# Performance work log

Hardware: AMD Instinct MI355X
Metric: run time of the kernel (lower is better)

## Reference

```python
import jax, jax.numpy as jnp
import numpy as np

N = 8192
IN_F = 256
OUT_F = 128


def setup_inputs() -> dict:
    key = jax.random.key(0)
    k1, k2, k3, k4, k5, k6 = jax.random.split(key, 6)
    input = jax.random.normal(k1, (N, IN_F), dtype=jnp.float32)
    adj = jax.random.randint(k2, (N, N), 0, 2, dtype=jnp.int32)
    # xavier-uniform-like init scaled by gain=0.5
    def xavier(k, shape, gain=0.5):
        fan_in, fan_out = shape[0], shape[1]
        lim = gain * np.sqrt(6.0 / (fan_in + fan_out))
        return jax.random.uniform(k, shape, dtype=jnp.float32, minval=-lim, maxval=lim)
    W_s = xavier(k3, (IN_F, OUT_F))
    a_s = xavier(k4, (OUT_F, 1))
    W_n = xavier(k5, (IN_F, OUT_F))
    a_n = xavier(k6, (OUT_F, 1))
    return {"input": input, "adj": adj, "W_s": W_s, "a_s": a_s, "W_n": W_n, "a_n": a_n}


def reference(input, adj, W_s, a_s, W_n, a_n):
    # Projections: [N, out_features]
    h_s = input @ W_s
    h_n = input @ W_n
    # Additive attention logits: e[i, j] = relu((h_s @ a_s)[i] + (h_n @ a_n)[j])
    e = jax.nn.relu((h_s @ a_s) + (h_n @ a_n).T)  # [N, N]
    # Masked softmax over neighbors (dim=1)
    attention = jnp.where(adj > 0, e, jnp.float32(-9e15))
    attention = jax.nn.softmax(attention, axis=1)
    # Self-scaling term (sum of softmax rows, kept for faithfulness)
    attention_sum = jnp.sum(attention, axis=-1, keepdims=True)
    attention_s = 1.0 / (1.0 + attention_sum)
    # Dropout is identity in eval mode (p=0 / training=False)
    h_prime = attention_s * h_s + attention @ h_n
    # concat=True -> elu activation
    return jax.nn.elu(h_prime)
```

## Files before the change

### kernel.cpp

```cpp
#include <hip/hip_runtime.h>
#include <math.h>

#define NN 8192

typedef short short8 __attribute__((ext_vector_type(8)));
typedef float f32x4 __attribute__((ext_vector_type(4)));

__device__ __forceinline__ float eluf(float x) {
  return x > 0.f ? x : (__expf(x) - 1.f);
}
__device__ __forceinline__ unsigned short f2bf(float f) {
  union { float f; unsigned u; } v; v.f = f;
  unsigned r = v.u + 0x7fffu + ((v.u >> 16) & 1u);
  return (unsigned short)(r >> 16);
}

__global__ __launch_bounds__(256) void k_proj(const float* __restrict__ X,
                                              const float* __restrict__ Ws,
                                              const float* __restrict__ Wn,
                                              const float* __restrict__ as_,
                                              const float* __restrict__ an_,
                                              float* __restrict__ Hs,
                                              unsigned short* __restrict__ HnT,
                                              float* __restrict__ s_out,
                                              float* __restrict__ n_out) {
  __shared__ float4 lin4[8 * 64];
  const int t = threadIdx.x;
  const int i0 = blockIdx.x * 8;
  const float4* Xg = (const float4*)X + (size_t)i0 * 64;
  lin4[t] = Xg[t];
  if (t < 256) lin4[t + 256] = Xg[t + 256];
  __syncthreads();
  const int c = t & 127;
  const int rh = t >> 7;
  float accs[4], accn[4];
#pragma unroll
  for (int r = 0; r < 4; ++r) { accs[r] = 0.f; accn[r] = 0.f; }
  for (int k = 0; k < 256; k += 4) {
    float ws0 = Ws[(k + 0) * 128 + c], ws1 = Ws[(k + 1) * 128 + c];
    float ws2 = Ws[(k + 2) * 128 + c], ws3 = Ws[(k + 3) * 128 + c];
    float wn0 = Wn[(k + 0) * 128 + c], wn1 = Wn[(k + 1) * 128 + c];
    float wn2 = Wn[(k + 2) * 128 + c], wn3 = Wn[(k + 3) * 128 + c];
#pragma unroll
    for (int r = 0; r < 4; ++r) {
      float4 iv = lin4[(rh * 4 + r) * 64 + (k >> 2)];
      accs[r] = fmaf(iv.x, ws0, accs[r]); accs[r] = fmaf(iv.y, ws1, accs[r]);
      accs[r] = fmaf(iv.z, ws2, accs[r]); accs[r] = fmaf(iv.w, ws3, accs[r]);
      accn[r] = fmaf(iv.x, wn0, accn[r]); accn[r] = fmaf(iv.y, wn1, accn[r]);
      accn[r] = fmaf(iv.z, wn2, accn[r]); accn[r] = fmaf(iv.w, wn3, accn[r]);
    }
  }
#pragma unroll
  for (int r = 0; r < 4; ++r)
    Hs[(size_t)(i0 + rh * 4 + r) * 128 + c] = accs[r];
  {
    union { unsigned short us[4]; ushort4 u4; } pk;
#pragma unroll
    for (int r = 0; r < 4; ++r) pk.us[r] = f2bf(accn[r]);
    *(ushort4*)(HnT + (size_t)c * NN + i0 + rh * 4) = pk.u4;
  }
  float* red = (float*)lin4;
  const int wv = t >> 6, ln = t & 63;
  __syncthreads();
  {
    float av = as_[c];
#pragma unroll
    for (int r = 0; r < 4; ++r) red[(rh * 4 + r) * 128 + c] = accs[r] * av;
  }
  __syncthreads();
#pragma unroll
  for (int h = 0; h < 2; ++h) {
    int row = wv * 2 + h;
    float p = red[row * 128 + ln] + red[row * 128 + 64 + ln];
#pragma unroll
    for (int off = 32; off >= 1; off >>= 1) p += __shfl_down(p, off);
    if (ln == 0) s_out[i0 + row] = p;
  }
  __syncthreads();
  {
    float av = an_[c];
#pragma unroll
    for (int r = 0; r < 4; ++r) red[(rh * 4 + r) * 128 + c] = accn[r] * av;
  }
  __syncthreads();
#pragma unroll
  for (int h = 0; h < 2; ++h) {
    int row = wv * 2 + h;
    float p = red[row * 128 + ln] + red[row * 128 + 64 + ln];
#pragma unroll
    for (int off = 32; off >= 1; off >>= 1) p += __shfl_down(p, off);
    if (ln == 0) n_out[i0 + row] = p;
  }
}

__global__ __launch_bounds__(256) void k_main(const int* __restrict__ A,
                                              const unsigned short* __restrict__ HnT,
                                              const float* __restrict__ sv_g,
                                              const float* __restrict__ nv_g,
                                              float* __restrict__ HsOut) {
  __shared__ short8 fragbuf[2][4][64];
  __shared__ float zsh[64];
  __shared__ float zf[16];

  const int t = threadIdx.x;
  const int wv = t >> 6;
  const int ln = t & 63;
  const int q = ln >> 4;
  const int m = ln & 15;
  const int row0 = blockIdx.x * 16;

  const float sm = sv_g[row0 + m];
  const int jlane = wv * 32 + q * 8;
  const int* aptr = A + (size_t)(row0 + m) * NN + jlane;
  const float* nptr = nv_g + jlane;

  const int f0 = wv * 32 + m;
  const unsigned short* bb0 = HnT + (size_t)f0 * NN + q * 8;
  const unsigned short* bb1 = HnT + (size_t)(f0 + 16) * NN + q * 8;

  f32x4 acc0 = {0.f, 0.f, 0.f, 0.f}, acc1 = {0.f, 0.f, 0.f, 0.f};
  float zp = 0.f;

  int4 adjv[2][2];
  float4 nvv[2][2];
  union { uint4 u; short8 s; } breg[8];
  adjv[0][0] = *(const int4*)(aptr);       adjv[0][1] = *(const int4*)(aptr + 4);
  adjv[1][0] = *(const int4*)(aptr + 128); adjv[1][1] = *(const int4*)(aptr + 132);
  nvv[0][0] = *(const float4*)(nptr);      nvv[0][1] = *(const float4*)(nptr + 4);
  breg[0].u = *(const uint4*)(bb0);        breg[1].u = *(const uint4*)(bb0 + 32);
  breg[2].u = *(const uint4*)(bb0 + 64);   breg[3].u = *(const uint4*)(bb0 + 96);
  breg[4].u = *(const uint4*)(bb1);        breg[5].u = *(const uint4*)(bb1 + 32);
  breg[6].u = *(const uint4*)(bb1 + 64);   breg[7].u = *(const uint4*)(bb1 + 96);

#pragma unroll 2
  for (int tt = 0; tt < 64; ++tt) {
    const int cur = tt & 1;
    {
      float nvl[8] = {nvv[cur][0].x, nvv[cur][0].y, nvv[cur][0].z, nvv[cur][0].w,
                      nvv[cur][1].x, nvv[cur][1].y, nvv[cur][1].z, nvv[cur][1].w};
      int av[8] = {adjv[cur][0].x, adjv[cur][0].y, adjv[cur][0].z, adjv[cur][0].w,
                   adjv[cur][1].x, adjv[cur][1].y, adjv[cur][1].z, adjv[cur][1].w};
      short8 fr;
#pragma unroll
      for (int k = 0; k < 8; ++k) {
        float w = av[k] > 0 ? __expf(fmaxf(sm + nvl[k], 0.f)) : 0.f;
        zp += w;
        fr[k] = (short)f2bf(w);
      }
      fragbuf[cur][wv][ln] = fr;
    }
    if (tt < 62) {
      const int* p = aptr + (tt + 2) * 128;
      adjv[cur][0] = *(const int4*)p;
      adjv[cur][1] = *(const int4*)(p + 4);
    }
    if (tt < 63) {
      const float* p = nptr + (tt + 1) * 128;
      nvv[cur ^ 1][0] = *(const float4*)p;
      nvv[cur ^ 1][1] = *(const float4*)(p + 4);
    }
    __syncthreads();
    short8 a0 = fragbuf[cur][0][ln];
    short8 a1 = fragbuf[cur][1][ln];
    short8 a2 = fragbuf[cur][2][ln];
    short8 a3 = fragbuf[cur][3][ln];
    acc0 = __builtin_amdgcn_mfma_f32_16x16x32_bf16(a0, breg[0].s, acc0, 0, 0, 0);
    acc1 = __builtin_amdgcn_mfma_f32_16x16x32_bf16(a0, breg[4].s, acc1, 0, 0, 0);
    acc0 = __builtin_amdgcn_mfma_f32_16x16x32_bf16(a1, breg[1].s, acc0, 0, 0, 0);
    acc1 = __builtin_amdgcn_mfma_f32_16x16x32_bf16(a1, breg[5].s, acc1, 0, 0, 0);
    acc0 = __builtin_amdgcn_mfma_f32_16x16x32_bf16(a2, breg[2].s, acc0, 0, 0, 0);
    acc1 = __builtin_amdgcn_mfma_f32_16x16x32_bf16(a2, breg[6].s, acc1, 0, 0, 0);
    acc0 = __builtin_amdgcn_mfma_f32_16x16x32_bf16(a3, breg[3].s, acc0, 0, 0, 0);
    acc1 = __builtin_amdgcn_mfma_f32_16x16x32_bf16(a3, breg[7].s, acc1, 0, 0, 0);
    if (tt < 63) {
      const size_t jt = (size_t)(tt + 1) * 128;
      breg[0].u = *(const uint4*)(bb0 + jt);      breg[1].u = *(const uint4*)(bb0 + jt + 32);
      breg[2].u = *(const uint4*)(bb0 + jt + 64); breg[3].u = *(const uint4*)(bb0 + jt + 96);
      breg[4].u = *(const uint4*)(bb1 + jt);      breg[5].u = *(const uint4*)(bb1 + jt + 32);
      breg[6].u = *(const uint4*)(bb1 + jt + 64); breg[7].u = *(const uint4*)(bb1 + jt + 96);
    }
  }

  {
    float zz = zp;
    zz += __shfl_down(zz, 32);
    zz += __shfl_down(zz, 16);
    if (ln < 16) zsh[wv * 16 + ln] = zz;
  }
  __syncthreads();
  if (t < 16) zf[t] = 1.f / (zsh[t] + zsh[16 + t] + zsh[32 + t] + zsh[48 + t]);
  __syncthreads();

#pragma unroll
  for (int reg = 0; reg < 4; ++reg) {
    const int row = q * 4 + reg;
    const float invz = zf[row];
    const size_t off = (size_t)(row0 + row) * 128 + f0;
    float h0 = HsOut[off], h1 = HsOut[off + 16];
    HsOut[off]      = eluf(fmaf(acc0[reg], invz, 0.5f * h0));
    HsOut[off + 16] = eluf(fmaf(acc1[reg], invz, 0.5f * h1));
  }
}

extern "C" void kernel_launch(void* const* d_in, const int* in_sizes, int n_in,
                              void* d_out, int out_size, void* d_ws, size_t ws_size,
                              hipStream_t stream) {
  const float* X   = (const float*)d_in[0];
  const int*   A   = (const int*)d_in[1];
  const float* Ws  = (const float*)d_in[2];
  const float* as_ = (const float*)d_in[3];
  const float* Wn  = (const float*)d_in[4];
  const float* an_ = (const float*)d_in[5];
  float* out = (float*)d_out;

  unsigned short* HnT = (unsigned short*)d_ws;
  float* s = (float*)(HnT + (size_t)128 * NN);
  float* n = s + NN;

  k_proj<<<1024, 256, 0, stream>>>(X, Ws, Wn, as_, an_, out, HnT, s, n);
  k_main<<<512, 256, 0, stream>>>(A, HnT, s, n, out);
}
```

Baseline: 464.6 us.

## Split neighbor dimension across waves with blocked HnT layout and LDS reduction

The attention-times-Hn product is now split along the neighbor (K) dimension instead of the feature dimension. Each of 8 waves covers a contiguous 1024-column slice of adj and computes all 128 output features with its own attention fragment, so the per-iteration LDS exchange and __syncthreads are gone. HnT is rewritten into a blocked 8-element-chunk layout so B-fragment loads are contiguous. Partial accumulators are then reduced across waves through a 64KB LDS buffer, and the block grows to 512 threads with s_setprio around the MFMAs. In exchange it uses more registers (8 accumulators) and a large LDS footprint that may limit occupancy.

```diff
diff --git a/kernel.cpp b/kernel.cpp
--- a/kernel.cpp
+++ b/kernel.cpp
@@ -57,7 +57,7 @@
     union { unsigned short us[4]; ushort4 u4; } pk;
 #pragma unroll
     for (int r = 0; r < 4; ++r) pk.us[r] = f2bf(accn[r]);
-    *(ushort4*)(HnT + (size_t)c * NN + i0 + rh * 4) = pk.u4;
+    *(ushort4*)(HnT + (size_t)blockIdx.x * 1024 + c * 8 + rh * 4) = pk.u4;
   }
   float* red = (float*)lin4;
   const int wv = t >> 6, ln = t & 63;
@@ -93,13 +93,13 @@
   }
 }
 
-__global__ __launch_bounds__(256) void k_main(const int* __restrict__ A,
-                                              const unsigned short* __restrict__ HnT,
-                                              const float* __restrict__ sv_g,
-                                              const float* __restrict__ nv_g,
-                                              float* __restrict__ HsOut) {
-  __shared__ short8 fragbuf[2][4][64];
-  __shared__ float zsh[64];
+__global__ __launch_bounds__(512, 4) void k_main(const int* __restrict__ A,
+                                                 const unsigned short* __restrict__ HnT,
+                                                 const float* __restrict__ sv_g,
+                                                 const float* __restrict__ nv_g,
+                                                 float* __restrict__ HsOut) {
+  __shared__ float accbuf[8][16][128];
+  __shared__ float zsh[8][16];
   __shared__ float zf[16];
 
   const int t = threadIdx.x;
@@ -110,74 +110,71 @@
   const int row0 = blockIdx.x * 16;
 
   const float sm = sv_g[row0 + m];
-  const int jlane = wv * 32 + q * 8;
-  const int* aptr = A + (size_t)(row0 + m) * NN + jlane;
-  const float* nptr = nv_g + jlane;
-
-  const int f0 = wv * 32 + m;
-  const unsigned short* bb0 = HnT + (size_t)f0 * NN + q * 8;
-  const unsigned short* bb1 = HnT + (size_t)(f0 + 16) * NN + q * 8;
-
-  f32x4 acc0 = {0.f, 0.f, 0.f, 0.f}, acc1 = {0.f, 0.f, 0.f, 0.f};
+  const int jbase = wv * 1024 + q * 8;
+  const int* aptr = A + (size_t)(row0 + m) * NN + jbase;
+  const float* nptr = nv_g + jbase;
+  const unsigned short* bptr = HnT + ((size_t)(wv * 128 + q) * 128 + m) * 8;
+
+  f32x4 acc[8];
+#pragma unroll
+  for (int ft = 0; ft < 8; ++ft) acc[ft] = (f32x4){0.f, 0.f, 0.f, 0.f};
   float zp = 0.f;
 
   int4 adjv[2][2];
   float4 nvv[2][2];
-  union { uint4 u; short8 s; } breg[8];
+  union Breg { uint4 u; short8 s; };
+  Breg breg[8];
+
   adjv[0][0] = *(const int4*)(aptr);       adjv[0][1] = *(const int4*)(aptr + 4);
-  adjv[1][0] = *(const int4*)(aptr + 128); adjv[1][1] = *(const int4*)(aptr + 132);
+  adjv[1][0] = *(const int4*)(aptr + 32);  adjv[1][1] = *(const int4*)(aptr + 36);
   nvv[0][0] = *(const float4*)(nptr);      nvv[0][1] = *(const float4*)(nptr + 4);
-  breg[0].u = *(const uint4*)(bb0);        breg[1].u = *(const uint4*)(bb0 + 32);
-  breg[2].u = *(const uint4*)(bb0 + 64);   breg[3].u = *(const uint4*)(bb0 + 96);
-  breg[4].u = *(const uint4*)(bb1);        breg[5].u = *(const uint4*)(bb1 + 32);
-  breg[6].u = *(const uint4*)(bb1 + 64);   breg[7].u = *(const uint4*)(bb1 + 96);
+  breg[0].u = *(const uint4*)(bptr);       breg[1].u = *(const uint4*)(bptr + 128);
+  breg[2].u = *(const uint4*)(bptr + 256); breg[3].u = *(const uint4*)(bptr + 384);
+  breg[4].u = *(const uint4*)(bptr + 512); breg[5].u = *(const uint4*)(bptr + 640);
+  breg[6].u = *(const uint4*)(bptr + 768); breg[7].u = *(const uint4*)(bptr + 896);
 
 #pragma unroll 2
-  for (int tt = 0; tt < 64; ++tt) {
+  for (int tt = 0; tt < 32; ++tt) {
     const int cur = tt & 1;
+    short8 fr;
     {
       float nvl[8] = {nvv[cur][0].x, nvv[cur][0].y, nvv[cur][0].z, nvv[cur][0].w,
                       nvv[cur][1].x, nvv[cur][1].y, nvv[cur][1].z, nvv[cur][1].w};
       int av[8] = {adjv[cur][0].x, adjv[cur][0].y, adjv[cur][0].z, adjv[cur][0].w,
                    adjv[cur][1].x, adjv[cur][1].y, adjv[cur][1].z, adjv[cur][1].w};
-      short8 fr;
 #pragma unroll
       for (int k = 0; k < 8; ++k) {
         float w = av[k] > 0 ? __expf(fmaxf(sm + nvl[k], 0.f)) : 0.f;
         zp += w;
         fr[k] = (short)f2bf(w);
       }
-      fragbuf[cur][wv][ln] = fr;
-    }
-    if (tt < 62) {
-      const int* p = aptr + (tt + 2) * 128;
+    }
+    if (tt < 31) {
+      const float* p = nptr + (tt + 1) * 32;
+      nvv[cur ^ 1][0] = *(const float4*)p;
+      nvv[cur ^ 1][1] = *(const float4*)(p + 4);
+    }
+    __builtin_amdgcn_s_setprio(1);
+    acc[0] = __builtin_amdgcn_mfma_f32_16x16x32_bf16(fr, breg[0].s, acc[0], 0, 0, 0);
+    acc[1] = __builtin_amdgcn_mfma_f32_16x16x32_bf16(fr, breg[1].s, acc[1], 0, 0, 0);
+    acc[2] = __builtin_amdgcn_mfma_f32_16x16x32_bf16(fr, breg[2].s, acc[2], 0, 0, 0);
+    acc[3] = __builtin_amdgcn_mfma_f32_16x16x32_bf16(fr, breg[3].s, acc[3], 0, 0, 0);
+    acc[4] = __builtin_amdgcn_mfma_f32_16x16x32_bf16(fr, breg[4].s, acc[4], 0, 0, 0);
+    acc[5] = __builtin_amdgcn_mfma_f32_16x16x32_bf16(fr, breg[5].s, acc[5], 0, 0, 0);
+    acc[6] = __builtin_amdgcn_mfma_f32_16x16x32_bf16(fr, breg[6].s, acc[6], 0, 0, 0);
+    acc[7] = __builtin_amdgcn_mfma_f32_16x16x32_bf16(fr, breg[7].s, acc[7], 0, 0, 0);
+    __builtin_amdgcn_s_setprio(0);
+    if (tt < 31) {
+      const unsigned short* p = bptr + (size_t)(tt + 1) * 4096;
+      breg[0].u = *(const uint4*)(p);       breg[1].u = *(const uint4*)(p + 128);
+      breg[2].u = *(const uint4*)(p + 256); breg[3].u = *(const uint4*)(p + 384);
+      breg[4].u = *(const uint4*)(p + 512); breg[5].u = *(const uint4*)(p + 640);
+      breg[6].u = *(const uint4*)(p + 768); breg[7].u = *(const uint4*)(p + 896);
+    }
+    if (tt < 30) {
+      const int* p = aptr + (tt + 2) * 32;
       adjv[cur][0] = *(const int4*)p;
       adjv[cur][1] = *(const int4*)(p + 4);
-    }
-    if (tt < 63) {
-      const float* p = nptr + (tt + 1) * 128;
-      nvv[cur ^ 1][0] = *(const float4*)p;
-      nvv[cur ^ 1][1] = *(const float4*)(p + 4);
-    }
-    __syncthreads();
-    short8 a0 = fragbuf[cur][0][ln];
-    short8 a1 = fragbuf[cur][1][ln];
-    short8 a2 = fragbuf[cur][2][ln];
-    short8 a3 = fragbuf[cur][3][ln];
-    acc0 = __builtin_amdgcn_mfma_f32_16x16x32_bf16(a0, breg[0].s, acc0, 0, 0, 0);
-    acc1 = __builtin_amdgcn_mfma_f32_16x16x32_bf16(a0, breg[4].s, acc1, 0, 0, 0);
-    acc0 = __builtin_amdgcn_mfma_f32_16x16x32_bf16(a1, breg[1].s, acc0, 0, 0, 0);
-    acc1 = __builtin_amdgcn_mfma_f32_16x16x32_bf16(a1, breg[5].s, acc1, 0, 0, 0);
-    acc0 = __builtin_amdgcn_mfma_f32_16x16x32_bf16(a2, breg[2].s, acc0, 0, 0, 0);
-    acc1 = __builtin_amdgcn_mfma_f32_16x16x32_bf16(a2, breg[6].s, acc1, 0, 0, 0);
-    acc0 = __builtin_amdgcn_mfma_f32_16x16x32_bf16(a3, breg[3].s, acc0, 0, 0, 0);
-    acc1 = __builtin_amdgcn_mfma_f32_16x16x32_bf16(a3, breg[7].s, acc1, 0, 0, 0);
-    if (tt < 63) {
-      const size_t jt = (size_t)(tt + 1) * 128;
-      breg[0].u = *(const uint4*)(bb0 + jt);      breg[1].u = *(const uint4*)(bb0 + jt + 32);
-      breg[2].u = *(const uint4*)(bb0 + jt + 64); breg[3].u = *(const uint4*)(bb0 + jt + 96);
-      breg[4].u = *(const uint4*)(bb1 + jt);      breg[5].u = *(const uint4*)(bb1 + jt + 32);
-      breg[6].u = *(const uint4*)(bb1 + jt + 64); breg[7].u = *(const uint4*)(bb1 + jt + 96);
     }
   }
 
@@ -185,20 +182,36 @@
     float zz = zp;
     zz += __shfl_down(zz, 32);
     zz += __shfl_down(zz, 16);
-    if (ln < 16) zsh[wv * 16 + ln] = zz;
-  }
-  __syncthreads();
-  if (t < 16) zf[t] = 1.f / (zsh[t] + zsh[16 + t] + zsh[32 + t] + zsh[48 + t]);
-  __syncthreads();
-
-#pragma unroll
-  for (int reg = 0; reg < 4; ++reg) {
-    const int row = q * 4 + reg;
+    if (ln < 16) zsh[wv][ln] = zz;
+  }
+#pragma unroll
+  for (int ft = 0; ft < 8; ++ft) {
+#pragma unroll
+    for (int reg = 0; reg < 4; ++reg)
+      accbuf[wv][q * 4 + reg][ft * 16 + m] = acc[ft][reg];
+  }
+  __syncthreads();
+  if (t < 16) {
+    float z = zsh[0][t] + zsh[1][t] + zsh[2][t] + zsh[3][t] +
+              zsh[4][t] + zsh[5][t] + zsh[6][t] + zsh[7][t];
+    zf[t] = 1.f / z;
+  }
+  __syncthreads();
+  {
+    const int row = t >> 5;
+    const int f0 = (t & 31) * 4;
+    f32x4 ssum = *(const f32x4*)&accbuf[0][row][f0];
+#pragma unroll
+    for (int w = 1; w < 8; ++w) ssum += *(const f32x4*)&accbuf[w][row][f0];
     const float invz = zf[row];
     const size_t off = (size_t)(row0 + row) * 128 + f0;
-    float h0 = HsOut[off], h1 = HsOut[off + 16];
-    HsOut[off]      = eluf(fmaf(acc0[reg], invz, 0.5f * h0));
-    HsOut[off + 16] = eluf(fmaf(acc1[reg], invz, 0.5f * h1));
+    float4 h = *(const float4*)(HsOut + off);
+    float4 o;
+    o.x = eluf(fmaf(ssum[0], invz, 0.5f * h.x));
+    o.y = eluf(fmaf(ssum[1], invz, 0.5f * h.y));
+    o.z = eluf(fmaf(ssum[2], invz, 0.5f * h.z));
+    o.w = eluf(fmaf(ssum[3], invz, 0.5f * h.w));
+    *(float4*)(HsOut + off) = o;
   }
 }
 
@@ -218,5 +231,5 @@
   float* n = s + NN;
 
   k_proj<<<1024, 256, 0, stream>>>(X, Ws, Wn, as_, an_, out, HnT, s, n);
-  k_main<<<512, 256, 0, stream>>>(A, HnT, s, n, out);
-}
+  k_main<<<512, 512, 0, stream>>>(A, HnT, s, n, out);
+}
```

Result: no change. 459.7 us (-1.1%).
